# Performance work log

Hardware: AMD Instinct MI355X
Metric: run time of the kernel (lower is better)

## Reference

```python
import jax, jax.numpy as jnp
import numpy as np

B = 2048   # windows per stream
N = 49     # tokens per 7x7 window
C = 192    # dim
H = 6      # heads
D = C // H # head_dim = 32
WH = WW = 7
SCALE = D ** -0.5


def _rel_pos_index():
    coords = np.stack(np.meshgrid(np.arange(WH), np.arange(WW), indexing='ij')).reshape(2, -1)
    rc = (coords[:, :, None] - coords[:, None, :]).transpose(1, 2, 0)  # [N,N,2]
    rc[..., 0] += WH - 1
    rc[..., 1] += WW - 1
    rc[..., 0] *= 2 * WW - 1
    return rc.sum(-1)  # [N,N] ints in [0, 169)

RPI = _rel_pos_index()


def setup_inputs() -> dict:
    key = jax.random.key(0)
    ks = jax.random.split(key, 16)
    w = lambda k, sh: jax.random.normal(k, sh, jnp.float32) * 0.02
    s = lambda v: jnp.asarray(v, jnp.float32)
    return {
        'x_sa': jax.random.normal(ks[0], (2 * B, N, C), jnp.float32),
        'x_ca': jax.random.normal(ks[1], (B, 2 * N, C), jnp.float32),
        'lambda_sa': s(0.1),
        'lambda_ca': s(0.1),
        'sa_enh': s(0.1),
        'ca_enh': s(0.1),
        'W_sa_qkv': w(ks[2], (C, 3 * C)), 'b_sa_qkv': jnp.zeros((3 * C,), jnp.float32),
        'W_sa_ct': w(ks[3], (C, C)), 'W_sa_cr': w(ks[4], (C, C)),
        'W_ca_q': w(ks[5], (C, C)), 'b_ca_q': jnp.zeros((C,), jnp.float32),
        'W_ca_kv': w(ks[6], (C, 2 * C)), 'b_ca_kv': jnp.zeros((2 * C,), jnp.float32),
        'W_ca_ct': w(ks[7], (C, C)), 'W_ca_cr': w(ks[8], (C, C)),
        'rpb_table': w(ks[9], ((2 * WH - 1) * (2 * WW - 1), H)),
        'W_proj_sa': w(ks[10], (C, C)), 'b_proj_sa': jnp.zeros((C,), jnp.float32),
        'W_proj_ca': w(ks[11], (C, C)), 'b_proj_ca': jnp.zeros((C,), jnp.float32),
    }


def _heads(x):  # [B,N,C] -> [B,H,N,D]
    b, n, _ = x.shape
    return x.reshape(b, n, H, D).transpose(0, 2, 1, 3)


def _merge(x):  # [B,H,N,D] -> [B,N,C]
    b = x.shape[0]
    return x.transpose(0, 2, 1, 3).reshape(b, -1, C)


def _diff_attn(qt, kt, vt, qr, kr, vr, bias, lam_param):
    at = jax.nn.softmax(jnp.einsum('bhnd,bhmd->bhnm', qt * SCALE, kt) + bias, axis=-1)
    ar = jax.nn.softmax(jnp.einsum('bhnd,bhmd->bhnm', qr * SCALE, kr) + bias, axis=-1)
    lam = jnp.clip(jax.nn.sigmoid(lam_param), 0.01, 0.99)
    ot = jnp.einsum('bhnm,bhmd->bhnd', at - lam * ar, vt)
    orf = jnp.einsum('bhnm,bhmd->bhnd', ar - lam * at, vr)
    return ot, orf


def _forward(x_sa, x_ca, lambda_sa, lambda_ca, sa_enh, ca_enh,
             W_sa_qkv, b_sa_qkv, W_sa_ct, W_sa_cr,
             W_ca_q, b_ca_q, W_ca_kv, b_ca_kv, W_ca_ct, W_ca_cr,
             rpb_table, W_proj_sa, b_proj_sa, W_proj_ca, b_proj_ca):
    bias = rpb_table[RPI.reshape(-1)].reshape(N, N, H).transpose(2, 0, 1)  # [H,N,N]

    # ---- self-attention path (streams concat on batch) ----
    xt, xr = x_sa[:B], x_sa[B:]
    te = xt + sa_enh * (xr @ W_sa_cr)
    re = xr + sa_enh * (xt @ W_sa_ct)
    qkv_t = (te @ W_sa_qkv + b_sa_qkv).reshape(B, N, 3, H, D).transpose(2, 0, 3, 1, 4)
    qkv_r = (re @ W_sa_qkv + b_sa_qkv).reshape(B, N, 3, H, D).transpose(2, 0, 3, 1, 4)
    ot, orf = _diff_attn(qkv_t[0], qkv_t[1], qkv_t[2], qkv_r[0], qkv_r[1], qkv_r[2], bias, lambda_sa)
    out_sa = jnp.concatenate([_merge(ot) @ W_proj_sa + b_proj_sa,
                              _merge(orf) @ W_proj_sa + b_proj_sa], axis=0)  # [2B,N,C]

    # ---- cross-attention path (streams concat on sequence) ----
    xt, xr = x_ca[:, :N, :], x_ca[:, N:, :]
    te = xt + ca_enh * (xr @ W_ca_cr)
    re = xr + ca_enh * (xt @ W_ca_ct)
    qt = _heads(te @ W_ca_q + b_ca_q)
    qr = _heads(re @ W_ca_q + b_ca_q)
    xcat = jnp.concatenate([te, re], axis=1)  # [B,2N,C]
    kv = (xcat @ W_ca_kv + b_ca_kv).reshape(B, 2 * N, 2, H, D).transpose(2, 0, 3, 1, 4)
    k, v = kv[0], kv[1]  # [B,H,2N,D]
    ot, orf = _diff_attn(qt, k[:, :, :N], v[:, :, :N], qr, k[:, :, N:], v[:, :, N:], bias, lambda_ca)
    out_ca = jnp.concatenate([_merge(ot) @ W_proj_ca + b_proj_ca,
                              _merge(orf) @ W_proj_ca + b_proj_ca], axis=1)  # [B,2N,C]

    return jnp.stack([out_sa, out_ca.reshape(2 * B, N, C)], axis=0)  # [2,2B,N,C]


def reference(x_sa, x_ca, lambda_sa, lambda_ca, sa_enh, ca_enh,
              W_sa_qkv, b_sa_qkv, W_sa_ct, W_sa_cr,
              W_ca_q, b_ca_q, W_ca_kv, b_ca_kv, W_ca_ct, W_ca_cr,
              rpb_table, W_proj_sa, b_proj_sa, W_proj_ca, b_proj_ca):
    return _forward(x_sa, x_ca, lambda_sa, lambda_ca, sa_enh, ca_enh,
                    W_sa_qkv, b_sa_qkv, W_sa_ct, W_sa_cr,
                    W_ca_q, b_ca_q, W_ca_kv, b_ca_kv, W_ca_ct, W_ca_cr,
                    rpb_table, W_proj_sa, b_proj_sa, W_proj_ca, b_proj_ca)
```

## Files before the change

kernel.cpp:

```cpp
#include <hip/hip_runtime.h>
#include <cmath>

static constexpr float SCALE_ = 0.17677669529663687f;

typedef __attribute__((ext_vector_type(8))) _Float16 f16x8;
typedef __attribute__((ext_vector_type(8))) ushort u16x8;
typedef __attribute__((ext_vector_type(4))) float f32x4;

__device__ inline ushort f16u(float f) {
    union { _Float16 h; ushort u; } c;
    c.h = (_Float16)f;
    return c.u;
}

__device__ __forceinline__ void gld16(const ushort* g, ushort* l) {
    __builtin_amdgcn_global_load_lds(
        (const __attribute__((address_space(1))) unsigned int*)g,
        (__attribute__((address_space(3))) unsigned int*)l,
        16, 0, 0);
}

struct SmallmmJobs {
    const float* Wa[6];
    const float* Wb[6];
    const float* sc[6];
    float*       out[6];
    int          NCb[6];
    int          base[7];
};
__global__ __launch_bounds__(256) void smallmm_all(SmallmmJobs J)
{
    int b = blockIdx.x;
    int j = 0;
    #pragma unroll
    for (int k = 1; k < 6; ++k) if (b >= J.base[k]) j = k;
    int idx = (b - J.base[j]) * 256 + threadIdx.x;
    int NCb = J.NCb[j];
    int n4  = NCb >> 2;
    int m   = idx / n4;
    int n0  = (idx - m * n4) << 2;
    if (m >= 192) return;
    const float* Wa = J.Wa[j];
    const float* Wb = J.Wb[j];
    float s = J.sc[j][0];
    float ax = 0.f, ay = 0.f, az = 0.f, aw = 0.f;
    for (int k = 0; k < 192; ++k) {
        float a = Wa[m * 192 + k];
        const float4 bv = *(const float4*)(Wb + (size_t)k * NCb + n0);
        ax += a * bv.x; ay += a * bv.y; az += a * bv.z; aw += a * bv.w;
    }
    float4 r = make_float4(ax * s, ay * s, az * s, aw * s);
    *(float4*)(J.out[j] + (size_t)m * NCb + n0) = r;
}

struct WtJobs {
    const float* W[11];
    ushort*      dh[11];
    int          NC[11];
    int          base[12];
};
__global__ __launch_bounds__(256) void conv_wT_all(WtJobs J)
{
    int b = blockIdx.x;
    int j = 0;
    #pragma unroll
    for (int k = 1; k < 11; ++k) if (b >= J.base[k]) j = k;
    int idx = (b - J.base[j]) * 256 + threadIdx.x;
    int NC = J.NC[j];
    if (idx >= NC * 192) return;
    int n = idx / 192, k = idx - n * 192;
    float f = J.W[j][(long long)k * NC + n];
    long long o = ((long long)(k >> 5) * NC + n) * 32 + (k & 31);
    J.dh[j][o] = f16u(f);
}

__global__ __launch_bounds__(256) void conv_x2(
    const float* __restrict__ src_t, const float* __restrict__ src_r,
    long long src_bs,
    ushort* __restrict__ dh_t, ushort* __restrict__ dh_r, int Mc)
{
    const long long SS = (long long)Mc * 32;
    const long long total8 = (long long)Mc * 24;
    for (long long t = (long long)blockIdx.x * 256 + threadIdx.x; t < 2 * total8;
         t += (long long)gridDim.x * 256) {
        const int second = (t >= total8);
        long long ti = second ? t - total8 : t;
        const float* src = second ? src_r : src_t;
        ushort* dh = second ? dh_r : dh_t;
        int m  = (int)(ti / 24);
        int c8 = (int)(ti - (long long)m * 24) * 8;
        int bb = m / 49, r = m - bb * 49;
        const float* sp = src + (long long)bb * src_bs + r * 192 + c8;
        float4 v0 = *(const float4*)sp;
        float4 v1 = *(const float4*)(sp + 4);
        float f[8] = {v0.x, v0.y, v0.z, v0.w, v1.x, v1.y, v1.z, v1.w};
        u16x8 h8;
        #pragma unroll
        for (int e = 0; e < 8; ++e) h8[e] = f16u(f[e]);
        long long o = (long long)(c8 >> 5) * SS + (long long)m * 32 + (c8 & 31);
        *(u16x8*)(dh + o) = h8;
    }
}

template<int NC, bool DUAL, bool F32OUT>
__global__ __launch_bounds__(256, 4) void gemm_f16(
    const ushort* __restrict__ A1a, const ushort* __restrict__ A2a,
    const ushort* __restrict__ B2a, ushort* __restrict__ outHa,
    float* __restrict__ outFa,
    const ushort* __restrict__ A1b, const ushort* __restrict__ A2b,
    const ushort* __restrict__ B2b, ushort* __restrict__ outHb,
    float* __restrict__ outFb,
    const ushort* __restrict__ B1, const float* __restrict__ bias,
    long long out_bs, int M)
{
    __shared__ __align__(16) ushort AHs[2][2048];
    __shared__ __align__(16) ushort BHs[2][6144];

    const int z = blockIdx.z;
    const ushort* Ah1 = z ? A1b : A1a;
    const ushort* Ah2 = z ? A2b : A2a;
    const ushort* Bh2 = z ? B2b : B2a;

    const int tid = threadIdx.x;
    const int lane = tid & 63, wv = tid >> 6;
    const int wm = (wv >> 1) * 32;
    const int wn = (wv & 1) * 96;
    const int lr = lane & 15, lg = lane >> 4;
    const int bn = blockIdx.x, bm = blockIdx.y;
    const long long SS = (long long)M * 32;
    constexpr int NP = DUAL ? 6 : 3;

    const int at_row = tid >> 2;
    const int at_c   = (tid & 3) ^ ((tid >> 3) & 3);
    const long long a_src = (long long)(bm * 64 + at_row) * 32 + at_c * 8;
    int b_src[3];
    #pragma unroll
    for (int k = 0; k < 3; ++k) {
        int t = k * 256 + tid;
        int row = t >> 2, c = (t & 3) ^ ((t >> 3) & 3);
        b_src[k] = (bn * 192 + row) * 32 + c * 8;
    }
    const int wdst = wv * 512;

    int aoff[2], boff[6];
    #pragma unroll
    for (int i = 0; i < 2; ++i) {
        int row = wm + 16 * i + lr;
        aoff[i] = (row * 4 + (lg ^ ((row >> 1) & 3))) * 8;
    }
    #pragma unroll
    for (int j = 0; j < 6; ++j) {
        int row = wn + 16 * j + lr;
        boff[j] = (row * 4 + (lg ^ ((row >> 1) & 3))) * 8;
    }

    f32x4 acc[2][6] = {};

    #pragma unroll
    for (int p = 0; p < NP; ++p) {
        #pragma unroll
        for (int hbf = 0; hbf < 2; ++hbf) {
            const int s = 2 * p + hbf;
            const int k6 = (s < 6) ? s : s - 6;
            const ushort* AHp = (!DUAL || s < 6) ? Ah1 : Ah2;
            const ushort* BHp = (!DUAL || s < 6) ? B1  : Bh2;
            const long long asb = (long long)k6 * SS;
            const int bsb = k6 * (NC * 32);
            gld16(AHp + asb + a_src, AHs[hbf] + wdst);
            #pragma unroll
            for (int k = 0; k < 3; ++k)
                gld16(BHp + bsb + b_src[k], BHs[hbf] + k * 2048 + wdst);
        }
        __syncthreads();

        #pragma unroll
        for (int hbf = 0; hbf < 2; ++hbf) {
            f16x8 ah[2];
            #pragma unroll
            for (int i = 0; i < 2; ++i)
                ah[i] = *(const f16x8*)&AHs[hbf][aoff[i]];
            #pragma unroll
            for (int j = 0; j < 6; ++j) {
                f16x8 bh = *(const f16x8*)&BHs[hbf][boff[j]];
                #pragma unroll
                for (int i = 0; i < 2; ++i)
                    acc[i][j] = __builtin_amdgcn_mfma_f32_16x16x32_f16(ah[i], bh, acc[i][j], 0, 0, 0);
            }
        }
        __syncthreads();
    }

    #pragma unroll
    for (int j = 0; j < 6; ++j) {
        const int c = bn * 192 + wn + 16 * j + lr;
        const float bv = bias ? bias[c] : 0.f;
        #pragma unroll
        for (int i = 0; i < 2; ++i)
            #pragma unroll
            for (int r = 0; r < 4; ++r) {
                int m = bm * 64 + wm + 16 * i + 4 * lg + r;
                if (m < M) {
                    float f = acc[i][j][r] + bv;
                    if constexpr (F32OUT) {
                        float* outF = z ? outFb : outFa;
                        int b2 = m / 49, r2 = m - b2 * 49;
                        outF[(long long)b2 * out_bs + r2 * 192 + c] = f;
                    } else {
                        ushort* outH = z ? outHb : outHa;
                        long long o = (long long)(c >> 5) * SS + (long long)m * 32 + (c & 31);
                        outH[o] = f16u(f);
                    }
                }
            }
    }
}

__global__ __launch_bounds__(256, 4) void attn_f16(
    const ushort* __restrict__ qT, const ushort* __restrict__ kT,
    const ushort* __restrict__ vT,
    const ushort* __restrict__ qR, const ushort* __restrict__ kR,
    const ushort* __restrict__ vR,
    long long SS,
    const float* __restrict__ rpb, const float* __restrict__ lam_ptr,
    ushort* __restrict__ otH, ushort* __restrict__ orH)
{
    __shared__ __align__(16) ushort Pth[64][72];
    __shared__ __align__(16) ushort Vs[2][32][70];
    __shared__ float bias_s[169];

    const int tid = threadIdx.x;
    const int bb = blockIdx.x / 6;
    const int h  = blockIdx.x - bb * 6;
    const int lane = tid & 63;
    const int w  = tid >> 6;
    const int li = lane & 15;
    const int lg = lane >> 4;
    const long long rowbase = (long long)bb * 49 * 32;
    const long long hb = (long long)h * SS + rowbase;

    for (int idx = tid; idx < 169; idx += 256) bias_s[idx] = rpb[idx * 6 + h];

    {
        const ushort* vsrc[2] = {vT + hb, vR + hb};
        for (int c = tid; c < 392; c += 256) {
            int s  = c / 196;
            int r2 = c - s * 196;
            int j  = r2 >> 2;
            int d4 = (r2 & 3) * 8;
            u16x8 v = *(const u16x8*)(vsrc[s] + j * 32 + d4);
            #pragma unroll
            for (int e = 0; e < 8; ++e) Vs[s][d4 + e][j] = v[e];
        }
        for (int c = tid; c < 2 * 32 * 21; c += 256) {
            int s  = c / (32 * 21);
            int r1 = c - s * (32 * 21);
            int d  = r1 / 21;
            int j  = 49 + (r1 - d * 21);
            Vs[s][d][j] = 0;
        }
    }

    float lraw = lam_ptr[0];
    float lam = 1.f / (1.f + __expf(-lraw));
    lam = fminf(fmaxf(lam, 0.01f), 0.99f);

    const int irow = min(w * 16 + li, 48);

    f32x4 st[2][4];
    #pragma unroll
    for (int s = 0; s < 2; ++s) {
        const ushort* qb = (s ? qR : qT) + hb;
        const ushort* kb = (s ? kR : kT) + hb;
        f16x8 qh = *(const f16x8*)(qb + irow * 32 + 8 * lg);
        #pragma unroll
        for (int jt = 0; jt < 4; ++jt) {
            int jr = jt * 16 + li; if (jr > 48) jr = 48;
            f16x8 kh = *(const f16x8*)(kb + jr * 32 + 8 * lg);
            f32x4 c = {};
            c = __builtin_amdgcn_mfma_f32_16x16x32_f16(kh, qh, c, 0, 0, 0);
            st[s][jt] = c;
        }
    }
    __syncthreads();

    const int ri = (irow * 9363) >> 16;
    const int ci = irow - 7 * ri;
    float bias_v[4][4];
    #pragma unroll
    for (int jt = 0; jt < 4; ++jt)
        #pragma unroll
        for (int r = 0; r < 4; ++r) {
            int j = jt * 16 + 4 * lg + r;
            int jc = (j < 49) ? j : 48;
            int rj = (jc * 9363) >> 16;
            int cj = jc - 7 * rj;
            bias_v[jt][r] = bias_s[(ri - rj + 6) * 13 + (ci - cj + 6)];
        }

    float p[2][4][4];
    #pragma unroll
    for (int s = 0; s < 2; ++s) {
        float m = -1e30f;
        #pragma unroll
        for (int jt = 0; jt < 4; ++jt)
            #pragma unroll
            for (int r = 0; r < 4; ++r) {
                int j = jt * 16 + 4 * lg + r;
                float sv = (j < 49) ? (st[s][jt][r] * SCALE_ + bias_v[jt][r]) : -1e30f;
                p[s][jt][r] = sv;
                m = fmaxf(m, sv);
            }
        m = fmaxf(m, __shfl_xor(m, 16));
        m = fmaxf(m, __shfl_xor(m, 32));
        float sum = 0.f;
        #pragma unroll
        for (int jt = 0; jt < 4; ++jt)
            #pragma unroll
            for (int r = 0; r < 4; ++r) {
                float e = __expf(p[s][jt][r] - m);
                p[s][jt][r] = e;
                sum += e;
            }
        sum += __shfl_xor(sum, 16);
        sum += __shfl_xor(sum, 32);
        float inv = 1.f / sum;
        #pragma unroll
        for (int jt = 0; jt < 4; ++jt)
            #pragma unroll
            for (int r = 0; r < 4; ++r)
                p[s][jt][r] *= inv;
    }

    const int prow = w * 16 + li;
    #pragma unroll
    for (int s = 0; s < 2; ++s) {
        #pragma unroll
        for (int jt = 0; jt < 4; ++jt) {
            ushort4 h4;
            #pragma unroll
            for (int r = 0; r < 4; ++r) {
                float at = p[0][jt][r], ar = p[1][jt][r];
                float f = (s == 0) ? (at - lam * ar) : (ar - lam * at);
                ((ushort*)&h4)[r] = f16u(f);
            }
            *(ushort4*)&Pth[prow][jt * 16 + 4 * lg] = h4;
        }

        f32x4 acc[2] = {};
        #pragma unroll
        for (int ks = 0; ks < 2; ++ks) {
            f16x8 pa = *(const f16x8*)&Pth[prow][ks * 32 + 8 * lg];
            #pragma unroll
            for (int dt = 0; dt < 2; ++dt) {
                f16x8 vh = *(const f16x8*)&Vs[s][dt * 16 + li][ks * 32 + 8 * lg];
                acc[dt] = __builtin_amdgcn_mfma_f32_16x16x32_f16(pa, vh, acc[dt], 0, 0, 0);
            }
        }
        ushort* oph = s ? orH : otH;
        #pragma unroll
        for (int dt = 0; dt < 2; ++dt)
            #pragma unroll
            for (int r = 0; r < 4; ++r) {
                int i = w * 16 + 4 * lg + r;
                if (i < 49) {
                    long long o = (long long)h * SS + rowbase + (long long)i * 32 + dt * 16 + li;
                    oph[o] = f16u(acc[dt][r]);
                }
            }
    }
}

extern "C" void kernel_launch(void* const* d_in, const int* in_sizes, int n_in,
                              void* d_out, int out_size, void* d_ws, size_t ws_size,
                              hipStream_t stream)
{
    const float* x_sa      = (const float*)d_in[0];
    const float* x_ca      = (const float*)d_in[1];
    const float* lam_sa    = (const float*)d_in[2];
    const float* lam_ca    = (const float*)d_in[3];
    const float* sa_enh    = (const float*)d_in[4];
    const float* ca_enh    = (const float*)d_in[5];
    const float* W_sa_qkv  = (const float*)d_in[6];
    const float* b_sa_qkv  = (const float*)d_in[7];
    const float* W_sa_ct   = (const float*)d_in[8];
    const float* W_sa_cr   = (const float*)d_in[9];
    const float* W_ca_q    = (const float*)d_in[10];
    const float* b_ca_q    = (const float*)d_in[11];
    const float* W_ca_kv   = (const float*)d_in[12];
    const float* b_ca_kv   = (const float*)d_in[13];
    const float* W_ca_ct   = (const float*)d_in[14];
    const float* W_ca_cr   = (const float*)d_in[15];
    const float* rpb       = (const float*)d_in[16];
    const float* W_proj_sa = (const float*)d_in[17];
    const float* b_proj_sa = (const float*)d_in[18];
    const float* W_proj_ca = (const float*)d_in[19];
    const float* b_proj_ca = (const float*)d_in[20];
    float* out = (float*)d_out;
    float* ws  = (float*)d_ws;

    float* CW0 = ws;
    float* CW1 = CW0 + 110592;
    float* CW2 = CW1 + 110592;
    float* CW3 = CW2 + 36864;
    float* CW4 = CW3 + 36864;
    float* CW5 = CW4 + 73728;

    {
        SmallmmJobs J;
        J.Wa[0]=W_sa_cr; J.Wb[0]=W_sa_qkv; J.sc[0]=sa_enh; J.out[0]=CW0; J.NCb[0]=576;
        J.Wa[1]=W_sa_ct; J.Wb[1]=W_sa_qkv; J.sc[1]=sa_enh; J.out[1]=CW1; J.NCb[1]=576;
        J.Wa[2]=W_ca_cr; J.Wb[2]=W_ca_q;   J.sc[2]=ca_enh; J.out[2]=CW2; J.NCb[2]=192;
        J.Wa[3]=W_ca_ct; J.Wb[3]=W_ca_q;   J.sc[3]=ca_enh; J.out[3]=CW3; J.NCb[3]=192;
        J.Wa[4]=W_ca_cr; J.Wb[4]=W_ca_kv;  J.sc[4]=ca_enh; J.out[4]=CW4; J.NCb[4]=384;
        J.Wa[5]=W_ca_ct; J.Wb[5]=W_ca_kv;  J.sc[5]=ca_enh; J.out[5]=CW5; J.NCb[5]=384;
        int bs[7] = {0,108,216,252,288,360,432};
        for (int i = 0; i < 7; ++i) J.base[i] = bs[i];
        smallmm_all<<<432, 256, 0, stream>>>(J);
    }

    ushort* wb = (ushort*)(ws + 442368);
    ushort* WsaqH = wb;
    ushort* C0H  = WsaqH + 110592;
    ushort* C1H  = C0H + 110592;
    ushort* WcqH = C1H + 110592;
    ushort* C2H  = WcqH + 36864;
    ushort* C3H  = C2H + 36864;
    ushort* WckH = C3H + 36864;
    ushort* C4H  = WckH + 73728;
    ushort* C5H  = C4H + 73728;
    ushort* WpsH = C5H + 73728;
    ushort* WpcH = WpsH + 36864;
    ushort* chunkU = WpcH + 36864;

    {
        WtJobs J;
        const float* Ws[11] = {W_sa_qkv, CW0, CW1, W_ca_q, CW2, CW3,
                               W_ca_kv, CW4, CW5, W_proj_sa, W_proj_ca};
        ushort* Ds[11] = {WsaqH, C0H, C1H, WcqH, C2H, C3H,
                          WckH, C4H, C5H, WpsH, WpcH};
        int NCs[11] = {576,576,576,192,192,192,384,384,384,192,192};
        int bs[12] = {0,432,864,1296,1440,1584,1728,2016,2304,2592,2736,2880};
        for (int i = 0; i < 11; ++i) { J.W[i]=Ws[i]; J.dh[i]=Ds[i]; J.NC[i]=NCs[i]; }
        for (int i = 0; i < 12; ++i) J.base[i] = bs[i];
        conv_wT_all<<<2880, 256, 0, stream>>>(J);
    }

    long long avail = (long long)ws_size - 442368LL * 4 - 737280LL * 2 - 65536;
    int cbmax = (int)(avail / 188160);
    if (cbmax > 2048) cbmax = 2048;
    if (cbmax < 1) cbmax = 1;

    const long long OUT1 = 2LL * 2048 * 49 * 192;
    dim3 blk(256);

    for (int c0 = 0; c0 < 2048; c0 += cbmax) {
        int cb = (c0 + cbmax <= 2048) ? cbmax : (2048 - c0);
        int M = cb * 49;
        long long SS = (long long)M * 32;
        int gy = (M + 63) / 64;
        int cblk = (int)(((long long)M * 48 + 255) / 256);
        if (cblk > 4096) cblk = 4096;

        dim3 g1(3, gy, 2), g2(1, gy, 2), g3(2, gy, 2);

        ushort* XtH = chunkU;
        ushort* XrH = XtH + (long long)cbmax * 9408;
        ushort* QtH = XrH + (long long)cbmax * 9408;
        ushort* QrH = QtH + (long long)cbmax * 28224;
        ushort* OtH = QrH + (long long)cbmax * 28224;
        ushort* OrH = OtH + (long long)cbmax * 9408;

        conv_x2<<<cblk, blk, 0, stream>>>(
            x_sa + (long long)c0 * 9408, x_sa + (2048LL + c0) * 9408, 9408,
            XtH, XrH, M);

        gemm_f16<576, true, false><<<g1, blk, 0, stream>>>(
            XtH, XrH, C0H, QtH, nullptr,
            XrH, XtH, C1H, QrH, nullptr,
            WsaqH, b_sa_qkv, 0, M);

        attn_f16<<<cb * 6, blk, 0, stream>>>(
            QtH, QtH + 6 * SS, QtH + 12 * SS,
            QrH, QrH + 6 * SS, QrH + 12 * SS,
            SS, rpb, lam_sa, OtH, OrH);

        gemm_f16<192, false, true><<<g2, blk, 0, stream>>>(
            OtH, nullptr, nullptr, nullptr, out + (long long)c0 * 9408,
            OrH, nullptr, nullptr, nullptr, out + (2048LL + c0) * 9408,
            WpsH, b_proj_sa, 9408, M);

        ushort* CXtH = chunkU;
        ushort* CXrH = CXtH + (long long)cbmax * 9408;
        ushort* CQtH = CXrH + (long long)cbmax * 9408;
        ushort* CQrH = CQtH + (long long)cbmax * 9408;
        ushort* KtH  = CQrH + (long long)cbmax * 9408;
        ushort* KrH  = KtH + (long long)cbmax * 18816;
        ushort* COtH = KrH + (long long)cbmax * 18816;
        ushort* COrH = COtH + (long long)cbmax * 9408;

        conv_x2<<<cblk, blk, 0, stream>>>(
            x_ca + (long long)c0 * 18816, x_ca + (long long)c0 * 18816 + 9408, 18816,
            CXtH, CXrH, M);

        gemm_f16<192, true, false><<<g2, blk, 0, stream>>>(
            CXtH, CXrH, C2H, CQtH, nullptr,
            CXrH, CXtH, C3H, CQrH, nullptr,
            WcqH, b_ca_q, 0, M);

        gemm_f16<384, true, false><<<g3, blk, 0, stream>>>(
            CXtH, CXrH, C4H, KtH, nullptr,
            CXrH, CXtH, C5H, KrH, nullptr,
            WckH, b_ca_kv, 0, M);

        attn_f16<<<cb * 6, blk, 0, stream>>>(
            CQtH, KtH, KtH + 6 * SS,
            CQrH, KrH, KrH + 6 * SS,
            SS, rpb, lam_ca, COtH, COrH);

        gemm_f16<192, false, true><<<g2, blk, 0, stream>>>(
            COtH, nullptr, nullptr, nullptr, out + OUT1 + (long long)c0 * 18816,
            COrH, nullptr, nullptr, nullptr, out + OUT1 + (long long)c0 * 18816 + 9408,
            WpcH, b_proj_ca, 18816, M);
    }
}
```

Measured before the change: 795.7 us.

## Software-pipeline GEMM K-loop with double buffering and XCD-aware block remap

The GEMM main loop changes from load-two-stages-then-compute to a rolling double buffer. Loads for stage s+2 are issued right after stage s is consumed, with s_waitcnt vmcnt(4) so global-to-LDS loads overlap the MFMA work. The 3D grid is flattened to 1D and remapped so consecutive logical tiles land on the same XCD (8-way round robin), aiming for better L2 reuse of the A/B tiles. The hand-written waitcnt depends on exactly four outstanding loads per stage, which is fragile if the compiler reorders memory operations.

```diff
diff --git a/kernel.cpp b/kernel.cpp
--- a/kernel.cpp
+++ b/kernel.cpp
@@ -116,7 +116,17 @@
     __shared__ __align__(16) ushort AHs[2][2048];
     __shared__ __align__(16) ushort BHs[2][6144];
 
-    const int z = blockIdx.z;
+    constexpr int GX = NC / 192;
+    const int nwg = gridDim.x;
+    const int orig = blockIdx.x;
+    const int q8 = nwg >> 3, r8b = nwg & 7;
+    const int xc = orig & 7, ix = orig >> 3;
+    const int L = (xc < r8b ? xc * (q8 + 1) : r8b * (q8 + 1) + (xc - r8b) * q8) + ix;
+    const int bm = L / (GX * 2);
+    const int rem = L - bm * (GX * 2);
+    const int bn = rem % GX;
+    const int z  = rem / GX;
+
     const ushort* Ah1 = z ? A1b : A1a;
     const ushort* Ah2 = z ? A2b : A2a;
     const ushort* Bh2 = z ? B2b : B2a;
@@ -126,9 +136,8 @@
     const int wm = (wv >> 1) * 32;
     const int wn = (wv & 1) * 96;
     const int lr = lane & 15, lg = lane >> 4;
-    const int bn = blockIdx.x, bm = blockIdx.y;
     const long long SS = (long long)M * 32;
-    constexpr int NP = DUAL ? 6 : 3;
+    constexpr int NS = DUAL ? 12 : 6;
 
     const int at_row = tid >> 2;
     const int at_c   = (tid & 3) ^ ((tid >> 3) & 3);
@@ -156,38 +165,43 @@
 
     f32x4 acc[2][6] = {};
 
-    #pragma unroll
-    for (int p = 0; p < NP; ++p) {
-        #pragma unroll
-        for (int hbf = 0; hbf < 2; ++hbf) {
-            const int s = 2 * p + hbf;
-            const int k6 = (s < 6) ? s : s - 6;
-            const ushort* AHp = (!DUAL || s < 6) ? Ah1 : Ah2;
-            const ushort* BHp = (!DUAL || s < 6) ? B1  : Bh2;
-            const long long asb = (long long)k6 * SS;
-            const int bsb = k6 * (NC * 32);
-            gld16(AHp + asb + a_src, AHs[hbf] + wdst);
-            #pragma unroll
-            for (int k = 0; k < 3; ++k)
-                gld16(BHp + bsb + b_src[k], BHs[hbf] + k * 2048 + wdst);
-        }
-        __syncthreads();
-
-        #pragma unroll
-        for (int hbf = 0; hbf < 2; ++hbf) {
-            f16x8 ah[2];
+    auto stage = [&](int buf, int s) {
+        const int k6 = (s < 6) ? s : s - 6;
+        const ushort* AHp = (!DUAL || s < 6) ? Ah1 : Ah2;
+        const ushort* BHp = (!DUAL || s < 6) ? B1  : Bh2;
+        const long long asb = (long long)k6 * SS;
+        const int bsb = k6 * (NC * 32);
+        gld16(AHp + asb + a_src, AHs[buf] + wdst);
+        #pragma unroll
+        for (int k = 0; k < 3; ++k)
+            gld16(BHp + bsb + b_src[k], BHs[buf] + k * 2048 + wdst);
+    };
+
+    stage(0, 0);
+    stage(1, 1);
+
+    #pragma unroll
+    for (int s = 0; s < NS; ++s) {
+        const int cur = s & 1;
+        if (s + 1 < NS) { asm volatile("s_waitcnt vmcnt(4)" ::: "memory"); }
+        else            { asm volatile("s_waitcnt vmcnt(0)" ::: "memory"); }
+        __builtin_amdgcn_s_barrier();
+        __builtin_amdgcn_sched_barrier(0);
+
+        f16x8 ah[2];
+        #pragma unroll
+        for (int i = 0; i < 2; ++i)
+            ah[i] = *(const f16x8*)&AHs[cur][aoff[i]];
+        #pragma unroll
+        for (int j = 0; j < 6; ++j) {
+            f16x8 bh = *(const f16x8*)&BHs[cur][boff[j]];
             #pragma unroll
             for (int i = 0; i < 2; ++i)
-                ah[i] = *(const f16x8*)&AHs[hbf][aoff[i]];
-            #pragma unroll
-            for (int j = 0; j < 6; ++j) {
-                f16x8 bh = *(const f16x8*)&BHs[hbf][boff[j]];
-                #pragma unroll
-                for (int i = 0; i < 2; ++i)
-                    acc[i][j] = __builtin_amdgcn_mfma_f32_16x16x32_f16(ah[i], bh, acc[i][j], 0, 0, 0);
-            }
-        }
-        __syncthreads();
+                acc[i][j] = __builtin_amdgcn_mfma_f32_16x16x32_f16(ah[i], bh, acc[i][j], 0, 0, 0);
+        }
+        __builtin_amdgcn_sched_barrier(0);
+        __builtin_amdgcn_s_barrier();
+        if (s + 2 < NS) stage(cur, s + 2);
     }
 
     #pragma unroll
@@ -461,7 +475,7 @@
         int cblk = (int)(((long long)M * 48 + 255) / 256);
         if (cblk > 4096) cblk = 4096;
 
-        dim3 g1(3, gy, 2), g2(1, gy, 2), g3(2, gy, 2);
+        dim3 g1(6 * gy), g2(2 * gy), g3(4 * gy);
 
         ushort* XtH = chunkU;
         ushort* XrH = XtH + (long long)cbmax * 9408;
```

After: 835.2 us. 1.05x slower.
